# Performance work log

Hardware: AMD Instinct MI355X
Metric: run time of the kernel (lower is better)

Reference implementation:

```python
import jax, jax.numpy as jnp
import numpy as np

L = 1024  # seq_len


def setup_inputs() -> dict:
    key = jax.random.key(0)
    ks = jax.random.split(key, 9)
    B = 4
    x = jax.random.uniform(ks[0], (B, L, L), dtype=jnp.float32)          # scores from pre_model
    M = (jax.random.uniform(ks[1], (B, L, L)) < 0.5).astype(jnp.float32)  # pairing-constraint mask
    M = M * M.transpose(0, 2, 1)  # symmetric binary mask
    return {
        "x": x,
        "M": M,
        "s": jnp.float32(0.5),
        "w": jax.random.uniform(ks[2], (1,), dtype=jnp.float32),
        "rho_p": jax.random.uniform(ks[3], (L, L), dtype=jnp.float32),
        "alpha": jnp.float32(0.005),
        "belt": jnp.float32(0.05),
        "lr_alpha": jnp.float32(0.99),
        "lr_belt": jnp.float32(0.99),
        "steps": 16,
    }


def _T_A(A_hat, M):
    # symmetrize then mask
    return (A_hat + A_hat.transpose(0, 2, 1)) * 0.5 * M


def reference(x, M, s, w, rho_p, alpha, belt, lr_alpha, lr_belt, steps):
    scores = x                      # pre_model output, [B, L, L]
    U = scores - s
    A_hat0 = scores
    A0 = _T_A(A_hat0, M)
    Lm0 = w * jax.nn.relu(jnp.sum(A0, axis=-1) - 1.0)   # [B, L] (w broadcasts)

    def step(carry, t):
        Lm, A, A_hat = carry
        # G = U/2 - Lm * sign(rowsum(A) - 1), broadcast over last dim
        row = jnp.sum(A, axis=-1) - 1.0                  # [B, L]
        G = U * 0.5 - (Lm * jnp.sign(row))[:, :, None]   # [B, L, L]
        at = alpha * jnp.power(lr_alpha, t)
        A_hat = A_hat + at * A_hat * M * (G + G.transpose(0, 2, 1))
        A_hat = jax.nn.relu(jnp.abs(A_hat) - rho_p * at)  # soft threshold
        A_hat = 1.0 - jax.nn.relu(1.0 - A_hat)            # clip above at 1
        A = _T_A(A_hat, M)
        Lm = Lm + belt * jnp.power(lr_belt, t) * jax.nn.relu(jnp.sum(A, axis=-1) - 1.0)
        return (Lm, A, A_hat), None

    ts = jnp.arange(steps, dtype=jnp.float32)
    (Lm, A, A_hat), _ = jax.lax.scan(step, (Lm0, A0, A_hat0), ts)
    return A
```

## Files before the change

### kernel.cpp

```cpp
#include <hip/hip_runtime.h>
#include <cstddef>
#include <math.h>

static constexpr int L = 1024;
static constexpr int B = 4;
static constexpr int NSTEPS = 16;
static constexpr int NTILE = 16;
static constexpr int NPAIR = NTILE * (NTILE + 1) / 2;
static constexpr int BL = B * L;

static constexpr size_t AH_OFF  = 0;
static constexpr size_t US_OFF  = (size_t)B * L * L;
static constexpr size_t CP_OFF  = 2 * (size_t)B * L * L;
static constexpr size_t RP0_OFF = CP_OFF + (size_t)B * 128 * L;
static constexpr size_t CP0_OFF = RP0_OFF + (size_t)B * 16 * L;
static constexpr size_t R_OFF   = CP0_OFF + (size_t)B * 16 * L;
static constexpr size_t LMA_OFF = R_OFF + (size_t)BL;
static constexpr size_t LMB_OFF = LMA_OFF + (size_t)BL;
static constexpr size_t CCA_OFF = LMB_OFF + (size_t)BL;
static constexpr size_t CCB_OFF = CCA_OFF + (size_t)BL;
static constexpr size_t SC_OFF  = CCB_OFF + (size_t)BL;
static constexpr size_t CTR_OFF = SC_OFF + 64;
static constexpr size_t CTR_U64 = 544;

__global__ __launch_bounds__(256) void init_kernel(
    const float* __restrict__ x, const float* __restrict__ M,
    const float* __restrict__ sp,
    float* __restrict__ ah, float* __restrict__ us,
    float* __restrict__ Rpart, float* __restrict__ Cpart0,
    unsigned long long* __restrict__ ctr64)
{
    __shared__ float lt[64][65];
    __shared__ float cpw[4][64];
    const int bid  = blockIdx.x;
    {
        const size_t gid = (size_t)bid * 256 + threadIdx.x;
        if (gid < CTR_U64) ctr64[gid] = 0ull;
    }
    const int chunk = bid & 7;
    const int rest  = bid >> 3;
    const int b  = rest >> 5;
    const int ti = (chunk << 1) | ((rest >> 4) & 1);
    const int tj = rest & 15;
    const int t  = threadIdx.x;
    const int w  = t >> 6;
    const int r  = t >> 4;
    const int c4 = (t & 15) << 2;
    const float s = sp[0];
    const float* xb = x + (size_t)b * L * L;

#pragma unroll
    for (int it = 0; it < 4; ++it) {
        int rr = r + 16 * it;
        float4 v = *(const float4*)(xb + (size_t)(tj * 64 + rr) * L + ti * 64 + c4);
        lt[rr][c4+0] = v.x; lt[rr][c4+1] = v.y; lt[rr][c4+2] = v.z; lt[rr][c4+3] = v.w;
    }
    __syncthreads();

    float cs0 = 0.f, cs1 = 0.f, cs2 = 0.f, cs3 = 0.f;
#pragma unroll
    for (int it = 0; it < 4; ++it) {
        int rr = r + 16 * it;
        int gi = ti * 64 + rr;
        size_t off = (size_t)b * L * L + (size_t)gi * L + tj * 64 + c4;
        float4 xv = *(const float4*)(x + off);
        float4 mv = *(const float4*)(M + off);
        *(float4*)(us + off) = make_float4(0.5f*(xv.x + lt[c4+0][rr]) - s,
                                           0.5f*(xv.y + lt[c4+1][rr]) - s,
                                           0.5f*(xv.z + lt[c4+2][rr]) - s,
                                           0.5f*(xv.w + lt[c4+3][rr]) - s);
        float a0 = xv.x*mv.x, a1 = xv.y*mv.y, a2 = xv.z*mv.z, a3 = xv.w*mv.w;
        *(float4*)(ah + off) = make_float4(a0, a1, a2, a3);
        float rs = (a0 + a1) + (a2 + a3);
        rs += __shfl_xor(rs, 1); rs += __shfl_xor(rs, 2);
        rs += __shfl_xor(rs, 4); rs += __shfl_xor(rs, 8);
        if ((t & 15) == 0) Rpart[((size_t)(b * 16 + tj)) * L + gi] = rs;
        cs0 += a0; cs1 += a1; cs2 += a2; cs3 += a3;
    }
    cs0 += __shfl_xor(cs0, 16); cs0 += __shfl_xor(cs0, 32);
    cs1 += __shfl_xor(cs1, 16); cs1 += __shfl_xor(cs1, 32);
    cs2 += __shfl_xor(cs2, 16); cs2 += __shfl_xor(cs2, 32);
    cs3 += __shfl_xor(cs3, 16); cs3 += __shfl_xor(cs3, 32);
    if ((t & 63) < 16) {
        int c0 = (t & 63) << 2;
        cpw[w][c0+0] = cs0; cpw[w][c0+1] = cs1; cpw[w][c0+2] = cs2; cpw[w][c0+3] = cs3;
    }
    __syncthreads();
    if (t < 64)
        Cpart0[((size_t)(b * 16 + ti)) * L + tj * 64 + t] =
            (cpw[0][t] + cpw[1][t]) + (cpw[2][t] + cpw[3][t]);
}

__global__ __launch_bounds__(256) void lminit_kernel(
    const float* __restrict__ wp,
    const float* __restrict__ alphap, const float* __restrict__ beltp,
    const float* __restrict__ lrap,  const float* __restrict__ lrbp,
    const float* __restrict__ Rpart, const float* __restrict__ Cpart0,
    float* __restrict__ Lm0, float* __restrict__ cc0, float* __restrict__ sc)
{
    const int bid = blockIdx.x;
    const int t   = threadIdx.x;
    if (bid == 0 && t < NSTEPS) {
        sc[t]          = alphap[0] * powf(lrap[0], (float)t);
        sc[NSTEPS + t] = beltp[0]  * powf(lrbp[0], (float)t);
    }
    const int b   = bid >> 2;
    const int i   = ((bid & 3) << 8) + t;
    float R0 = 0.f, C0 = 0.f;
#pragma unroll
    for (int k = 0; k < 16; ++k) {
        R0 += Rpart[((size_t)(b * 16 + k)) * L + i];
        C0 += Cpart0[((size_t)(b * 16 + k)) * L + i];
    }
    float rowv = 0.5f * (R0 + C0) - 1.0f;
    float rl = fmaxf(rowv, 0.f);
    float lm = wp[0] * rl;
    Lm0[b * L + i] = lm;
    float sg = (rowv > 0.f) ? 1.f : ((rowv < 0.f) ? -1.f : 0.f);
    cc0[b * L + i] = lm * sg;
}

__device__ __forceinline__ float step_elem(float a, float u, float rho,
                                           float ci, float cj, float at) {
    float g = u - ci - cj;
    float v = a * (1.f + at * g);
    v = fmaxf(fabsf(v) - rho * at, 0.f);
    return fminf(v, 1.f);
}

template <bool DO_SUMS>
__global__ __launch_bounds__(512) void update_kernel(
    const float* __restrict__ rho, const float* __restrict__ sc,
    float* __restrict__ ah, const float* __restrict__ us,
    const float* __restrict__ cc_in,
    const float* __restrict__ lm_in, float* __restrict__ lm_out,
    float* __restrict__ cc_out,
    float* __restrict__ Cpart, float* __restrict__ Rrow,
    unsigned int* __restrict__ ctr, int p)
{
    __shared__ float cp[8][1024];
    const int bid   = blockIdx.x;
    const int chunk = bid & 7;
    const int rest  = bid >> 3;
    const int b     = rest >> 4;
    const int slab  = (chunk << 4) | (rest & 15);
    const int t    = threadIdx.x;
    const int w    = t >> 6;
    const int l    = t & 63;
    const int row  = (slab << 3) + w;
    const size_t rowoff = (size_t)b * L * L + (size_t)row * L;
    const float at = sc[p];
    const float* ccb = cc_in + b * L;

    float4 cj[4];
#pragma unroll
    for (int k = 0; k < 4; ++k)
        cj[k] = *(const float4*)(ccb + k * 256 + l * 4);
    const float ci = ccb[row];

    float4 a4[4], u4[4], h4[4];
#pragma unroll
    for (int k = 0; k < 4; ++k) {
        const size_t off = rowoff + k * 256 + l * 4;
        a4[k] = *(const float4*)(ah + off);
        u4[k] = *(const float4*)(us + off);
        h4[k] = *(const float4*)(rho + (size_t)row * L + k * 256 + l * 4);
    }
#pragma unroll
    for (int k = 0; k < 4; ++k) {
        a4[k].x = step_elem(a4[k].x, u4[k].x, h4[k].x, ci, cj[k].x, at);
        a4[k].y = step_elem(a4[k].y, u4[k].y, h4[k].y, ci, cj[k].y, at);
        a4[k].z = step_elem(a4[k].z, u4[k].z, h4[k].z, ci, cj[k].z, at);
        a4[k].w = step_elem(a4[k].w, u4[k].w, h4[k].w, ci, cj[k].w, at);
        *(float4*)(ah + rowoff + k * 256 + l * 4) = a4[k];
    }

    if (DO_SUMS) {
        float rs = 0.f;
#pragma unroll
        for (int k = 0; k < 4; ++k)
            rs += (a4[k].x + a4[k].y) + (a4[k].z + a4[k].w);
        rs += __shfl_xor(rs, 1);  rs += __shfl_xor(rs, 2);  rs += __shfl_xor(rs, 4);
        rs += __shfl_xor(rs, 8);  rs += __shfl_xor(rs, 16); rs += __shfl_xor(rs, 32);
        if (l == 0)
            __hip_atomic_store(&Rrow[b * L + row], rs,
                               __ATOMIC_RELAXED, __HIP_MEMORY_SCOPE_AGENT);

#pragma unroll
        for (int k = 0; k < 4; ++k)
            *(float4*)&cp[w][k * 256 + l * 4] = a4[k];
        __syncthreads();
        const int c0 = t * 2;
        float2 acc = make_float2(0.f, 0.f);
#pragma unroll
        for (int j = 0; j < 8; ++j) {
            float2 v = *(float2*)&cp[j][c0];
            acc.x += v.x; acc.y += v.y;
        }
        {
            unsigned long long* cp64 =
                (unsigned long long*)(Cpart + ((size_t)(b * 128 + slab)) * L);
            union { float2 f; unsigned long long u; } pk; pk.f = acc;
            __hip_atomic_store(&cp64[t], pk.u,
                               __ATOMIC_RELAXED, __HIP_MEMORY_SCOPE_AGENT);
        }

        __syncthreads();
        const int rgrp = slab >> 3;
        unsigned int* gctr = ctr + ((b << 4) | rgrp) * 16;
        unsigned int* root = ctr + 1024 + (b << 4);
        if (t == 0) {
            unsigned old = __hip_atomic_fetch_add(gctr, 1u, __ATOMIC_RELAXED,
                                                  __HIP_MEMORY_SCOPE_AGENT);
            if (old == (unsigned)(p * 8 + 7))
                __hip_atomic_fetch_add(root, 1u, __ATOMIC_RELAXED,
                                       __HIP_MEMORY_SCOPE_AGENT);
        }

        if ((slab & 7) == 0) {
            if (t == 0) {
                const unsigned target = (unsigned)(p + 1) * 16u;
                while (__hip_atomic_load(root, __ATOMIC_RELAXED,
                                         __HIP_MEMORY_SCOPE_AGENT) < target)
                    __builtin_amdgcn_s_sleep(1);
            }
            __syncthreads();
            const int i  = slab >> 3;
            const int g  = t >> 5;
            const int cpair = t & 31;
            float sx = 0.f, sy = 0.f;
#pragma unroll
            for (int k = g * 8; k < g * 8 + 8; ++k) {
                const unsigned long long* q =
                    (const unsigned long long*)(Cpart + ((size_t)(b * 128 + k)) * L);
                unsigned long long raw = __hip_atomic_load(
                    &q[i * 32 + cpair], __ATOMIC_RELAXED, __HIP_MEMORY_SCOPE_AGENT);
                union { unsigned long long u; float2 f; } pk; pk.u = raw;
                sx += pk.f.x; sy += pk.f.y;
            }
            float* red = &cp[0][0];
            red[g * 64 + cpair * 2]     = sx;
            red[g * 64 + cpair * 2 + 1] = sy;
            __syncthreads();
            if (t < 64) {
                float tot = 0.f;
#pragma unroll
                for (int g2 = 0; g2 < 16; ++g2) tot += red[g2 * 64 + t];
                const int col = i * 64 + t;
                float Rv = __hip_atomic_load(&Rrow[b * L + col],
                                             __ATOMIC_RELAXED,
                                             __HIP_MEMORY_SCOPE_AGENT);
                float rowv = 0.5f * (Rv + tot) - 1.0f;
                float lm = lm_in[b * L + col] + sc[NSTEPS + p] * fmaxf(rowv, 0.f);
                lm_out[b * L + col] = lm;
                cc_out[b * L + col] =
                    lm * ((rowv > 0.f) ? 1.f : ((rowv < 0.f) ? -1.f : 0.f));
            }
        }
    }
}

__device__ __forceinline__ void decode_pair(int p, int& ti, int& tj) {
    int t = 0;
    while (p >= NTILE - t) { p -= NTILE - t; ++t; }
    ti = t; tj = t + p;
}

__global__ __launch_bounds__(256) void updfinal_kernel(
    const float* __restrict__ rho, const float* __restrict__ sc,
    const float* __restrict__ ah, const float* __restrict__ us,
    const float* __restrict__ ccf, float* __restrict__ out)
{
    __shared__ float la[64][65];
    __shared__ float lb[64][65];
    __shared__ float uu[64][65];
    const int task = blockIdx.x;
    const int b = task / NPAIR;
    int ti, tj; decode_pair(task % NPAIR, ti, tj);
    const int t  = threadIdx.x;
    const int r0 = t >> 4;
    const int c0 = (t & 15) << 2;
    const float at = sc[NSTEPS - 1];
    const float* ccb = ccf + b * L;
    const float* ahb = ah  + (size_t)b * L * L;
    const float* usb = us  + (size_t)b * L * L;
    float* ob        = out + (size_t)b * L * L;

    {
        float4 cjv = *(const float4*)(ccb + tj * 64 + c0);
        for (int it = 0; it < 4; ++it) {
            int r = r0 + 16 * it;
            int gi = ti * 64 + r;
            size_t off = (size_t)gi * L + tj * 64 + c0;
            float4 av = *(const float4*)(ahb + off);
            float4 uv = *(const float4*)(usb + off);
            float4 hv = *(const float4*)(rho + off);
            float ci = ccb[gi];
            la[r][c0+0] = step_elem(av.x, uv.x, hv.x, ci, cjv.x, at);
            la[r][c0+1] = step_elem(av.y, uv.y, hv.y, ci, cjv.y, at);
            la[r][c0+2] = step_elem(av.z, uv.z, hv.z, ci, cjv.z, at);
            la[r][c0+3] = step_elem(av.w, uv.w, hv.w, ci, cjv.w, at);
            uu[r][c0+0] = uv.x; uu[r][c0+1] = uv.y;
            uu[r][c0+2] = uv.z; uu[r][c0+3] = uv.w;
        }
    }
    __syncthreads();
    if (ti != tj) {
        float4 cjv = *(const float4*)(ccb + ti * 64 + c0);
        for (int it = 0; it < 4; ++it) {
            int r = r0 + 16 * it;
            int gi = tj * 64 + r;
            size_t off = (size_t)gi * L + ti * 64 + c0;
            float4 av = *(const float4*)(ahb + off);
            float4 hv = *(const float4*)(rho + off);
            float ci = ccb[gi];
            lb[r][c0+0] = step_elem(av.x, uu[c0+0][r], hv.x, ci, cjv.x, at);
            lb[r][c0+1] = step_elem(av.y, uu[c0+1][r], hv.y, ci, cjv.y, at);
            lb[r][c0+2] = step_elem(av.z, uu[c0+2][r], hv.z, ci, cjv.z, at);
            lb[r][c0+3] = step_elem(av.w, uu[c0+3][r], hv.w, ci, cjv.w, at);
        }
    }
    __syncthreads();

    for (int it = 0; it < 4; ++it) {
        int r = r0 + 16 * it;
        size_t off = (size_t)(ti * 64 + r) * L + tj * 64 + c0;
        float tb0, tb1, tb2, tb3;
        if (ti == tj) { tb0 = la[c0+0][r]; tb1 = la[c0+1][r]; tb2 = la[c0+2][r]; tb3 = la[c0+3][r]; }
        else          { tb0 = lb[c0+0][r]; tb1 = lb[c0+1][r]; tb2 = lb[c0+2][r]; tb3 = lb[c0+3][r]; }
        *(float4*)(ob + off) = make_float4(0.5f*(la[r][c0+0]+tb0), 0.5f*(la[r][c0+1]+tb1),
                                           0.5f*(la[r][c0+2]+tb2), 0.5f*(la[r][c0+3]+tb3));
    }
    if (ti != tj) {
        for (int it = 0; it < 4; ++it) {
            int r = r0 + 16 * it;
            size_t off = (size_t)(tj * 64 + r) * L + ti * 64 + c0;
            *(float4*)(ob + off) = make_float4(0.5f*(lb[r][c0+0]+la[c0+0][r]),
                                               0.5f*(lb[r][c0+1]+la[c0+1][r]),
                                               0.5f*(lb[r][c0+2]+la[c0+2][r]),
                                               0.5f*(lb[r][c0+3]+la[c0+3][r]));
        }
    }
}

extern "C" void kernel_launch(void* const* d_in, const int* in_sizes, int n_in,
                              void* d_out, int out_size, void* d_ws, size_t ws_size,
                              hipStream_t stream) {
    const float* x     = (const float*)d_in[0];
    const float* M     = (const float*)d_in[1];
    const float* s     = (const float*)d_in[2];
    const float* w     = (const float*)d_in[3];
    const float* rho   = (const float*)d_in[4];
    const float* alpha = (const float*)d_in[5];
    const float* belt  = (const float*)d_in[6];
    const float* lra   = (const float*)d_in[7];
    const float* lrb   = (const float*)d_in[8];
    float* out = (float*)d_out;

    float* ws     = (float*)d_ws;
    float* ah     = ws + AH_OFF;
    float* us     = ws + US_OFF;
    float* Cpart  = ws + CP_OFF;
    float* Rpart  = ws + RP0_OFF;
    float* Cpart0 = ws + CP0_OFF;
    float* Rrow   = ws + R_OFF;
    float* Lmb[2] = { ws + LMA_OFF, ws + LMB_OFF };
    float* ccb2[2] = { ws + CCA_OFF, ws + CCB_OFF };
    float* sc     = ws + SC_OFF;
    unsigned int* ctr = (unsigned int*)(ws + CTR_OFF);

    init_kernel<<<dim3(1024), dim3(256), 0, stream>>>(
        x, M, s, ah, us, Rpart, Cpart0, (unsigned long long*)ctr);
    lminit_kernel<<<dim3(16), dim3(256), 0, stream>>>(
        w, alpha, belt, lra, lrb, Rpart, Cpart0, Lmb[0], ccb2[0], sc);

    for (int p = 0; p < NSTEPS - 1; ++p) {
        update_kernel<true><<<dim3(512), dim3(512), 0, stream>>>(
            rho, sc, ah, us, ccb2[p & 1], Lmb[p & 1], Lmb[(p + 1) & 1],
            ccb2[(p + 1) & 1], Cpart, Rrow, ctr, p);
    }
    updfinal_kernel<<<dim3(B * NPAIR), dim3(256), 0, stream>>>(
        rho, sc, ah, us, ccb2[(NSTEPS - 1) & 1], out);
}
```

Baseline: 302.4 us.

## Move Lagrange multiplier reduction to start of next update kernel

Removes the tail-of-kernel cross-block counter/spin reduction that computed Lm and cc, and the separate lminit kernel. Each update kernel now has designated blocks reduce the previous step's column partials and publish cc. Other blocks spin on a per-step flag after issuing their loads for A_hat, U and rho, so the wait overlaps with those loads. Schedule scalars are computed inline with powf instead of a precomputed table. This relies on all blocks being co-resident for the in-kernel spin wait, and the flag array must be zeroed each call.

```diff
diff --git a/kernel.cpp b/kernel.cpp
--- a/kernel.cpp
+++ b/kernel.cpp
@@ -15,27 +15,24 @@
 static constexpr size_t RP0_OFF = CP_OFF + (size_t)B * 128 * L;
 static constexpr size_t CP0_OFF = RP0_OFF + (size_t)B * 16 * L;
 static constexpr size_t R_OFF   = CP0_OFF + (size_t)B * 16 * L;
-static constexpr size_t LMA_OFF = R_OFF + (size_t)BL;
-static constexpr size_t LMB_OFF = LMA_OFF + (size_t)BL;
-static constexpr size_t CCA_OFF = LMB_OFF + (size_t)BL;
-static constexpr size_t CCB_OFF = CCA_OFF + (size_t)BL;
-static constexpr size_t SC_OFF  = CCB_OFF + (size_t)BL;
-static constexpr size_t CTR_OFF = SC_OFF + 64;
-static constexpr size_t CTR_U64 = 544;
+static constexpr size_t LM_OFF  = R_OFF + (size_t)BL;
+static constexpr size_t CC_OFF  = LM_OFF + (size_t)BL;
+static constexpr size_t FLG_OFF = CC_OFF + (size_t)BL;
+static constexpr size_t FLG_U64 = 512;
 
 __global__ __launch_bounds__(256) void init_kernel(
     const float* __restrict__ x, const float* __restrict__ M,
     const float* __restrict__ sp,
     float* __restrict__ ah, float* __restrict__ us,
     float* __restrict__ Rpart, float* __restrict__ Cpart0,
-    unsigned long long* __restrict__ ctr64)
+    unsigned long long* __restrict__ flg64)
 {
     __shared__ float lt[64][65];
     __shared__ float cpw[4][64];
     const int bid  = blockIdx.x;
     {
         const size_t gid = (size_t)bid * 256 + threadIdx.x;
-        if (gid < CTR_U64) ctr64[gid] = 0ull;
+        if (gid < FLG_U64) flg64[gid] = 0ull;
     }
     const int chunk = bid & 7;
     const int rest  = bid >> 3;
@@ -91,35 +88,6 @@
             (cpw[0][t] + cpw[1][t]) + (cpw[2][t] + cpw[3][t]);
 }
 
-__global__ __launch_bounds__(256) void lminit_kernel(
-    const float* __restrict__ wp,
-    const float* __restrict__ alphap, const float* __restrict__ beltp,
-    const float* __restrict__ lrap,  const float* __restrict__ lrbp,
-    const float* __restrict__ Rpart, const float* __restrict__ Cpart0,
-    float* __restrict__ Lm0, float* __restrict__ cc0, float* __restrict__ sc)
-{
-    const int bid = blockIdx.x;
-    const int t   = threadIdx.x;
-    if (bid == 0 && t < NSTEPS) {
-        sc[t]          = alphap[0] * powf(lrap[0], (float)t);
-        sc[NSTEPS + t] = beltp[0]  * powf(lrbp[0], (float)t);
-    }
-    const int b   = bid >> 2;
-    const int i   = ((bid & 3) << 8) + t;
-    float R0 = 0.f, C0 = 0.f;
-#pragma unroll
-    for (int k = 0; k < 16; ++k) {
-        R0 += Rpart[((size_t)(b * 16 + k)) * L + i];
-        C0 += Cpart0[((size_t)(b * 16 + k)) * L + i];
-    }
-    float rowv = 0.5f * (R0 + C0) - 1.0f;
-    float rl = fmaxf(rowv, 0.f);
-    float lm = wp[0] * rl;
-    Lm0[b * L + i] = lm;
-    float sg = (rowv > 0.f) ? 1.f : ((rowv < 0.f) ? -1.f : 0.f);
-    cc0[b * L + i] = lm * sg;
-}
-
 __device__ __forceinline__ float step_elem(float a, float u, float rho,
                                            float ci, float cj, float at) {
     float g = u - ci - cj;
@@ -128,17 +96,24 @@
     return fminf(v, 1.f);
 }
 
-template <bool DO_SUMS>
+__device__ __forceinline__ float signf(float v) {
+    return (v > 0.f) ? 1.f : ((v < 0.f) ? -1.f : 0.f);
+}
+
+template <bool FIRST>
 __global__ __launch_bounds__(512) void update_kernel(
-    const float* __restrict__ rho, const float* __restrict__ sc,
+    const float* __restrict__ rho,
+    const float* __restrict__ alphap, const float* __restrict__ lrap,
+    const float* __restrict__ beltp,  const float* __restrict__ lrbp,
+    const float* __restrict__ wp,
     float* __restrict__ ah, const float* __restrict__ us,
-    const float* __restrict__ cc_in,
-    const float* __restrict__ lm_in, float* __restrict__ lm_out,
-    float* __restrict__ cc_out,
+    const float* __restrict__ Rpart, const float* __restrict__ Cpart0,
     float* __restrict__ Cpart, float* __restrict__ Rrow,
-    unsigned int* __restrict__ ctr, int p)
+    float* __restrict__ Lm, float* __restrict__ cc,
+    unsigned int* __restrict__ flags, int p)
 {
     __shared__ float cp[8][1024];
+    __shared__ float cpr[8][64];
     const int bid   = blockIdx.x;
     const int chunk = bid & 7;
     const int rest  = bid >> 3;
@@ -149,14 +124,6 @@
     const int l    = t & 63;
     const int row  = (slab << 3) + w;
     const size_t rowoff = (size_t)b * L * L + (size_t)row * L;
-    const float at = sc[p];
-    const float* ccb = cc_in + b * L;
-
-    float4 cj[4];
-#pragma unroll
-    for (int k = 0; k < 4; ++k)
-        cj[k] = *(const float4*)(ccb + k * 256 + l * 4);
-    const float ci = ccb[row];
 
     float4 a4[4], u4[4], h4[4];
 #pragma unroll
@@ -166,6 +133,64 @@
         u4[k] = *(const float4*)(us + off);
         h4[k] = *(const float4*)(rho + (size_t)row * L + k * 256 + l * 4);
     }
+
+    const float at = alphap[0] * powf(lrap[0], (float)p);
+    unsigned int* flag = flags + ((p << 2) | b) * 16;
+
+    if ((slab & 7) == 0) {
+        const int rcol0 = (slab >> 3) << 6;
+        float sv = 0.f;
+        if (FIRST) {
+#pragma unroll
+            for (int k = 2 * w; k < 2 * w + 2; ++k)
+                sv += Rpart[((size_t)(b * 16 + k)) * L + rcol0 + l]
+                    + Cpart0[((size_t)(b * 16 + k)) * L + rcol0 + l];
+        } else {
+#pragma unroll
+            for (int k = w * 16; k < w * 16 + 16; ++k)
+                sv += Cpart[((size_t)(b * 128 + k)) * L + rcol0 + l];
+        }
+        cpr[w][l] = sv;
+        __syncthreads();
+        if (w == 0) {
+            float tot = 0.f;
+#pragma unroll
+            for (int j = 0; j < 8; ++j) tot += cpr[j][l];
+            const int col = rcol0 + l;
+            float rowv, lm;
+            if (FIRST) {
+                rowv = 0.5f * tot - 1.0f;
+                lm = wp[0] * fmaxf(rowv, 0.f);
+            } else {
+                rowv = 0.5f * (Rrow[b * L + col] + tot) - 1.0f;
+                lm = Lm[b * L + col] +
+                     beltp[0] * powf(lrbp[0], (float)(p - 1)) * fmaxf(rowv, 0.f);
+            }
+            Lm[b * L + col] = lm;
+            __hip_atomic_store(&cc[b * L + col], lm * signf(rowv),
+                               __ATOMIC_RELAXED, __HIP_MEMORY_SCOPE_AGENT);
+            if (l == 0)
+                __hip_atomic_fetch_add(flag, 1u, __ATOMIC_RELEASE,
+                                       __HIP_MEMORY_SCOPE_AGENT);
+        }
+    }
+
+    if (t == 0) {
+        while (__hip_atomic_load(flag, __ATOMIC_RELAXED,
+                                 __HIP_MEMORY_SCOPE_AGENT) < 16u)
+            __builtin_amdgcn_s_sleep(1);
+        (void)__hip_atomic_load(flag, __ATOMIC_ACQUIRE,
+                                __HIP_MEMORY_SCOPE_AGENT);
+    }
+    __syncthreads();
+
+    const float* ccb = cc + b * L;
+    float4 cj[4];
+#pragma unroll
+    for (int k = 0; k < 4; ++k)
+        cj[k] = *(const float4*)(ccb + k * 256 + l * 4);
+    const float ci = ccb[row];
+
 #pragma unroll
     for (int k = 0; k < 4; ++k) {
         a4[k].x = step_elem(a4[k].x, u4[k].x, h4[k].x, ci, cj[k].x, at);
@@ -175,89 +200,26 @@
         *(float4*)(ah + rowoff + k * 256 + l * 4) = a4[k];
     }
 
-    if (DO_SUMS) {
-        float rs = 0.f;
-#pragma unroll
-        for (int k = 0; k < 4; ++k)
-            rs += (a4[k].x + a4[k].y) + (a4[k].z + a4[k].w);
-        rs += __shfl_xor(rs, 1);  rs += __shfl_xor(rs, 2);  rs += __shfl_xor(rs, 4);
-        rs += __shfl_xor(rs, 8);  rs += __shfl_xor(rs, 16); rs += __shfl_xor(rs, 32);
-        if (l == 0)
-            __hip_atomic_store(&Rrow[b * L + row], rs,
-                               __ATOMIC_RELAXED, __HIP_MEMORY_SCOPE_AGENT);
-
-#pragma unroll
-        for (int k = 0; k < 4; ++k)
-            *(float4*)&cp[w][k * 256 + l * 4] = a4[k];
-        __syncthreads();
-        const int c0 = t * 2;
-        float2 acc = make_float2(0.f, 0.f);
-#pragma unroll
-        for (int j = 0; j < 8; ++j) {
-            float2 v = *(float2*)&cp[j][c0];
-            acc.x += v.x; acc.y += v.y;
-        }
-        {
-            unsigned long long* cp64 =
-                (unsigned long long*)(Cpart + ((size_t)(b * 128 + slab)) * L);
-            union { float2 f; unsigned long long u; } pk; pk.f = acc;
-            __hip_atomic_store(&cp64[t], pk.u,
-                               __ATOMIC_RELAXED, __HIP_MEMORY_SCOPE_AGENT);
-        }
-
-        __syncthreads();
-        const int rgrp = slab >> 3;
-        unsigned int* gctr = ctr + ((b << 4) | rgrp) * 16;
-        unsigned int* root = ctr + 1024 + (b << 4);
-        if (t == 0) {
-            unsigned old = __hip_atomic_fetch_add(gctr, 1u, __ATOMIC_RELAXED,
-                                                  __HIP_MEMORY_SCOPE_AGENT);
-            if (old == (unsigned)(p * 8 + 7))
-                __hip_atomic_fetch_add(root, 1u, __ATOMIC_RELAXED,
-                                       __HIP_MEMORY_SCOPE_AGENT);
-        }
-
-        if ((slab & 7) == 0) {
-            if (t == 0) {
-                const unsigned target = (unsigned)(p + 1) * 16u;
-                while (__hip_atomic_load(root, __ATOMIC_RELAXED,
-                                         __HIP_MEMORY_SCOPE_AGENT) < target)
-                    __builtin_amdgcn_s_sleep(1);
-            }
-            __syncthreads();
-            const int i  = slab >> 3;
-            const int g  = t >> 5;
-            const int cpair = t & 31;
-            float sx = 0.f, sy = 0.f;
-#pragma unroll
-            for (int k = g * 8; k < g * 8 + 8; ++k) {
-                const unsigned long long* q =
-                    (const unsigned long long*)(Cpart + ((size_t)(b * 128 + k)) * L);
-                unsigned long long raw = __hip_atomic_load(
-                    &q[i * 32 + cpair], __ATOMIC_RELAXED, __HIP_MEMORY_SCOPE_AGENT);
-                union { unsigned long long u; float2 f; } pk; pk.u = raw;
-                sx += pk.f.x; sy += pk.f.y;
-            }
-            float* red = &cp[0][0];
-            red[g * 64 + cpair * 2]     = sx;
-            red[g * 64 + cpair * 2 + 1] = sy;
-            __syncthreads();
-            if (t < 64) {
-                float tot = 0.f;
-#pragma unroll
-                for (int g2 = 0; g2 < 16; ++g2) tot += red[g2 * 64 + t];
-                const int col = i * 64 + t;
-                float Rv = __hip_atomic_load(&Rrow[b * L + col],
-                                             __ATOMIC_RELAXED,
-                                             __HIP_MEMORY_SCOPE_AGENT);
-                float rowv = 0.5f * (Rv + tot) - 1.0f;
-                float lm = lm_in[b * L + col] + sc[NSTEPS + p] * fmaxf(rowv, 0.f);
-                lm_out[b * L + col] = lm;
-                cc_out[b * L + col] =
-                    lm * ((rowv > 0.f) ? 1.f : ((rowv < 0.f) ? -1.f : 0.f));
-            }
-        }
-    }
+    float rs = 0.f;
+#pragma unroll
+    for (int k = 0; k < 4; ++k)
+        rs += (a4[k].x + a4[k].y) + (a4[k].z + a4[k].w);
+    rs += __shfl_xor(rs, 1);  rs += __shfl_xor(rs, 2);  rs += __shfl_xor(rs, 4);
+    rs += __shfl_xor(rs, 8);  rs += __shfl_xor(rs, 16); rs += __shfl_xor(rs, 32);
+    if (l == 0) Rrow[b * L + row] = rs;
+
+#pragma unroll
+    for (int k = 0; k < 4; ++k)
+        *(float4*)&cp[w][k * 256 + l * 4] = a4[k];
+    __syncthreads();
+    const int c0 = t * 2;
+    float2 acc = make_float2(0.f, 0.f);
+#pragma unroll
+    for (int j = 0; j < 8; ++j) {
+        float2 v = *(float2*)&cp[j][c0];
+        acc.x += v.x; acc.y += v.y;
+    }
+    *(float2*)(Cpart + ((size_t)(b * 128 + slab)) * L + c0) = acc;
 }
 
 __device__ __forceinline__ void decode_pair(int p, int& ti, int& tj) {
@@ -267,21 +229,62 @@
 }
 
 __global__ __launch_bounds__(256) void updfinal_kernel(
-    const float* __restrict__ rho, const float* __restrict__ sc,
+    const float* __restrict__ rho,
+    const float* __restrict__ alphap, const float* __restrict__ lrap,
+    const float* __restrict__ beltp,  const float* __restrict__ lrbp,
     const float* __restrict__ ah, const float* __restrict__ us,
-    const float* __restrict__ ccf, float* __restrict__ out)
+    const float* __restrict__ Cpart, const float* __restrict__ Rrow,
+    const float* __restrict__ Lm, float* __restrict__ cc,
+    unsigned int* __restrict__ flags, float* __restrict__ out)
 {
     __shared__ float la[64][65];
     __shared__ float lb[64][65];
     __shared__ float uu[64][65];
+    __shared__ float cpr[4][64];
     const int task = blockIdx.x;
     const int b = task / NPAIR;
-    int ti, tj; decode_pair(task % NPAIR, ti, tj);
+    const int pairidx = task % NPAIR;
+    int ti, tj; decode_pair(pairidx, ti, tj);
     const int t  = threadIdx.x;
+    const int w  = t >> 6;
+    const int l  = t & 63;
+    const int p  = NSTEPS - 1;
+    const float at = alphap[0] * powf(lrap[0], (float)p);
+    unsigned int* flag = flags + ((p << 2) | b) * 16;
+
+    if (pairidx < 16) {
+        const int rcol0 = pairidx << 6;
+        float sv = 0.f;
+#pragma unroll
+        for (int k = w * 32; k < w * 32 + 32; ++k)
+            sv += Cpart[((size_t)(b * 128 + k)) * L + rcol0 + l];
+        cpr[w][l] = sv;
+        __syncthreads();
+        if (w == 0) {
+            float tot = (cpr[0][l] + cpr[1][l]) + (cpr[2][l] + cpr[3][l]);
+            const int col = rcol0 + l;
+            float rowv = 0.5f * (Rrow[b * L + col] + tot) - 1.0f;
+            float lm = Lm[b * L + col] +
+                       beltp[0] * powf(lrbp[0], (float)(p - 1)) * fmaxf(rowv, 0.f);
+            __hip_atomic_store(&cc[b * L + col], lm * signf(rowv),
+                               __ATOMIC_RELAXED, __HIP_MEMORY_SCOPE_AGENT);
+            if (l == 0)
+                __hip_atomic_fetch_add(flag, 1u, __ATOMIC_RELEASE,
+                                       __HIP_MEMORY_SCOPE_AGENT);
+        }
+    }
+    if (t == 0) {
+        while (__hip_atomic_load(flag, __ATOMIC_RELAXED,
+                                 __HIP_MEMORY_SCOPE_AGENT) < 16u)
+            __builtin_amdgcn_s_sleep(1);
+        (void)__hip_atomic_load(flag, __ATOMIC_ACQUIRE,
+                                __HIP_MEMORY_SCOPE_AGENT);
+    }
+    __syncthreads();
+
     const int r0 = t >> 4;
     const int c0 = (t & 15) << 2;
-    const float at = sc[NSTEPS - 1];
-    const float* ccb = ccf + b * L;
+    const float* ccb = cc + b * L;
     const float* ahb = ah  + (size_t)b * L * L;
     const float* usb = us  + (size_t)b * L * L;
     float* ob        = out + (size_t)b * L * L;
@@ -364,21 +367,21 @@
     float* Rpart  = ws + RP0_OFF;
     float* Cpart0 = ws + CP0_OFF;
     float* Rrow   = ws + R_OFF;
-    float* Lmb[2] = { ws + LMA_OFF, ws + LMB_OFF };
-    float* ccb2[2] = { ws + CCA_OFF, ws + CCB_OFF };
-    float* sc     = ws + SC_OFF;
-    unsigned int* ctr = (unsigned int*)(ws + CTR_OFF);
+    float* Lm     = ws + LM_OFF;
+    float* cc     = ws + CC_OFF;
+    unsigned int* flags = (unsigned int*)(ws + FLG_OFF);
 
     init_kernel<<<dim3(1024), dim3(256), 0, stream>>>(
-        x, M, s, ah, us, Rpart, Cpart0, (unsigned long long*)ctr);
-    lminit_kernel<<<dim3(16), dim3(256), 0, stream>>>(
-        w, alpha, belt, lra, lrb, Rpart, Cpart0, Lmb[0], ccb2[0], sc);
-
-    for (int p = 0; p < NSTEPS - 1; ++p) {
-        update_kernel<true><<<dim3(512), dim3(512), 0, stream>>>(
-            rho, sc, ah, us, ccb2[p & 1], Lmb[p & 1], Lmb[(p + 1) & 1],
-            ccb2[(p + 1) & 1], Cpart, Rrow, ctr, p);
+        x, M, s, ah, us, Rpart, Cpart0, (unsigned long long*)flags);
+
+    update_kernel<true><<<dim3(512), dim3(512), 0, stream>>>(
+        rho, alpha, lra, belt, lrb, w, ah, us, Rpart, Cpart0,
+        Cpart, Rrow, Lm, cc, flags, 0);
+    for (int p = 1; p < NSTEPS - 1; ++p) {
+        update_kernel<false><<<dim3(512), dim3(512), 0, stream>>>(
+            rho, alpha, lra, belt, lrb, w, ah, us, Rpart, Cpart0,
+            Cpart, Rrow, Lm, cc, flags, p);
     }
     updfinal_kernel<<<dim3(B * NPAIR), dim3(256), 0, stream>>>(
-        rho, sc, ah, us, ccb2[(NSTEPS - 1) & 1], out);
-}
+        rho, alpha, lra, belt, lrb, ah, us, Cpart, Rrow, Lm, cc, flags, out);
+}
```

After: 402.5 us. 33.1% more time.
